# Kernel tuning notes

Hardware: AMD Instinct MI355X
Metric: run time of the kernel (lower is better)

The kernel has to match this reference:

```python
import jax, jax.numpy as jnp
import numpy as np

N_QUBITS = 20
N_BLOCKS = 3
C64 = jnp.complex64


def _u3(theta, phi, lam):
    # U3(theta, phi, lam) = [[cos(t/2), -e^{i lam} sin(t/2)],
    #                        [e^{i phi} sin(t/2), e^{i(phi+lam)} cos(t/2)]]
    ct = jnp.cos(theta / 2).astype(C64)
    st = jnp.sin(theta / 2).astype(C64)
    el = jnp.exp(1j * lam.astype(C64))
    ep = jnp.exp(1j * phi.astype(C64))
    return jnp.stack([jnp.stack([ct, -el * st]),
                      jnp.stack([ep * st, ep * el * ct])])


def _cu3(theta, phi, lam):
    # controlled-U3: identity on control=|0>, U3 on control=|1>
    u = _u3(theta, phi, lam)
    m = jnp.zeros((4, 4), C64)
    m = m.at[:2, :2].set(jnp.eye(2, dtype=C64))
    m = m.at[2:, 2:].set(u)
    return m


def _apply1(psi, m, q):
    # psi: (2,)*N_QUBITS complex state tensor; apply 2x2 gate on qubit q
    psi = jnp.moveaxis(psi, q, 0).reshape(2, -1)
    psi = m @ psi
    return jnp.moveaxis(psi.reshape((2,) * N_QUBITS), 0, q)


def _apply2(psi, m4, c, t):
    # apply 4x4 gate on (control c, target t)
    psi = jnp.moveaxis(psi, (c, t), (0, 1)).reshape(4, -1)
    psi = m4 @ psi
    return jnp.moveaxis(psi.reshape((2,) * N_QUBITS), (0, 1), (c, t))


def _forward(u3_params, cu3_params):
    psi = jnp.zeros((2,) * N_QUBITS, C64).at[(0,) * N_QUBITS].set(1.0)
    for k in range(N_BLOCKS):
        for q in range(N_QUBITS):
            psi = _apply1(psi, _u3(*u3_params[k, q]), q)
        for q in range(N_QUBITS):  # circular CU3 ring: (q, (q+1) % n)
            psi = _apply2(psi, _cu3(*cu3_params[k, q]), q, (q + 1) % N_QUBITS)
    probs = (jnp.abs(psi) ** 2).reshape(2 ** N_QUBITS, 1)
    easy_scale_coeff = 2.0 ** (N_QUBITS - 1)
    gamma, beta, alpha = 0.1, 0.8, 0.3
    x = (beta * jnp.tanh(gamma * easy_scale_coeff * probs)) ** alpha
    return x - jnp.mean(x)


def setup_inputs() -> dict:
    key = jax.random.key(0)
    k1, k2 = jax.random.split(key)
    u3_params = jax.random.normal(k1, (N_BLOCKS, N_QUBITS, 3), dtype=jnp.float32)
    cu3_params = jax.random.normal(k2, (N_BLOCKS, N_QUBITS, 3), dtype=jnp.float32)
    return {"u3_params": u3_params, "cu3_params": cu3_params}


def reference(u3_params, cu3_params):
    return _forward(u3_params, cu3_params)
```

## Files before the change

kernel.cpp:

```cpp
#include <hip/hip_runtime.h>
#include <cstdint>
#include <cstddef>


#define NB 512
#define NT 512
#define SW(i) ((i) ^ (((i) >> 3) & 1u))

__device__ __forceinline__ float2 cmadd2(float2 m0, float2 a0, float2 m1, float2 a1) {
  float2 r;
  r.x = m0.x * a0.x - m0.y * a0.y + m1.x * a1.x - m1.y * a1.y;
  r.y = m0.x * a0.y + m0.y * a0.x + m1.x * a1.y + m1.y * a1.x;
  return r;
}
__device__ __forceinline__ float2 cmul(float2 a, float2 b) {
  return make_float2(a.x * b.x - a.y * b.y, a.x * b.y + a.y * b.x);
}
__device__ __forceinline__ float2 cadd(float2 a, float2 b) {
  return make_float2(a.x + b.x, a.y + b.y);
}

__device__ __forceinline__ void applyU3b0(float2* v, const float2* m) {
  float2 m00 = m[0], m01 = m[1], m10 = m[2], m11 = m[3];
  float2 a0 = v[0], a1 = v[1];
  v[0] = cmadd2(m00, a0, m01, a1); v[1] = cmadd2(m10, a0, m11, a1);
  a0 = v[2]; a1 = v[3];
  v[2] = cmadd2(m00, a0, m01, a1); v[3] = cmadd2(m10, a0, m11, a1);
}
__device__ __forceinline__ void applyF(float2* v, const float2* W0, const float2* W1) {
  float2 a0 = v[0], a1 = v[2];
  v[0] = cmadd2(W0[0], a0, W0[1], a1); v[2] = cmadd2(W0[2], a0, W0[3], a1);
  a0 = v[1]; a1 = v[3];
  v[1] = cmadd2(W1[0], a0, W1[1], a1); v[3] = cmadd2(W1[2], a0, W1[3], a1);
}
__device__ __forceinline__ void applyC(float2* v, const float2* u) {
  float2 a0 = v[1], a1 = v[3];
  v[1] = cmadd2(u[0], a0, u[1], a1); v[3] = cmadd2(u[2], a0, u[3], a1);
}

__device__ __forceinline__ float xval(float2 a) {
  float p = a.x * a.x + a.y * a.y;
  return powf(0.8f * tanhf(52428.8f * p), 0.3f);
}

__device__ __forceinline__ void mat_from(const float* s, float2* m) {
  float st, ct, sl, cl, sp, cp, spl, cpl;
  sincosf(0.5f * s[0], &st, &ct);
  sincosf(s[2], &sl, &cl);
  sincosf(s[1], &sp, &cp);
  sincosf(s[1] + s[2], &spl, &cpl);
  m[0] = make_float2(ct, 0.f);
  m[1] = make_float2(-cl * st, -sl * st);
  m[2] = make_float2(cp * st, sp * st);
  m[3] = make_float2(cpl * ct, spl * ct);
}

template <int TYPE, int INIT, int FINAL>
__global__ __launch_bounds__(NT, 4) void pass_k(const float* __restrict__ u3p,
                                                const float* __restrict__ cu3p, int k,
                                                const float2* __restrict__ in,
                                                float2* __restrict__ outPsi,
                                                float* __restrict__ accum,
                                                float* __restrict__ out) {
  __shared__ float4 A4[1024], B4[1024];
  __shared__ float2 M[168];
  __shared__ float red[8];
  unsigned t = threadIdx.x, b = blockIdx.x;

  float2 v[4];
  if (INIT) {
    v[0] = v[1] = v[2] = v[3] = make_float2(0.f, 0.f);
    if (b == 0 && t == 0) { v[0] = make_float2(1.f, 0.f); *accum = 0.f; }
  } else {
    const float4* in4 = (const float4*)in;
    unsigned F0 = ((t & 255u) << 11) + 2u * (t >> 8) + 4u * (b & 255u) + (b >> 8);
    float4 f0 = in4[F0];
    float4 f1 = in4[F0 + 1024u];
    v[0] = make_float2(f0.x, f0.y); v[1] = make_float2(f0.z, f0.w);
    v[2] = make_float2(f1.x, f1.y); v[3] = make_float2(f1.z, f1.w);
  }

  float2* MU = M;
  float2* MC = M + 80;
  if (t < 20) {
    mat_from(u3p + (k * 20 + t) * 3, MU + 4 * t);
  } else if (t >= 64 && t < 84) {
    unsigned c = t - 64;
    float2 u[4];
    mat_from(cu3p + (k * 20 + c) * 3, u);
    if (c == 19) {
      MC[76] = u[0]; MC[77] = u[1]; MC[78] = u[2]; MC[79] = u[3];
    } else {
      float2 ut[4];
      mat_from(u3p + (k * 20 + c + 1) * 3, ut);
      MC[4 * c + 0] = cadd(cmul(u[0], ut[0]), cmul(u[1], ut[2]));
      MC[4 * c + 1] = cadd(cmul(u[0], ut[1]), cmul(u[1], ut[3]));
      MC[4 * c + 2] = cadd(cmul(u[2], ut[0]), cmul(u[3], ut[2]));
      MC[4 * c + 3] = cadd(cmul(u[2], ut[1]), cmul(u[3], ut[3]));
    }
  }
  __syncthreads();

#pragma unroll
  for (int p = 0; p < 10; ++p) {
    if (TYPE == 0) {
      if (p == 0) applyU3b0(v, MU);
      applyF(v, MU + 4 * (p + 1), MC + 4 * p);
    } else {
      if (p < 9) applyF(v, MU + 4 * (11 + p), MC + 4 * (10 + p));
      else       applyC(v, MC + 4 * 19);
    }
    if (p < 9) {
      float4* buf = (p & 1) ? B4 : A4;
      buf[SW(t)]        = make_float4(v[0].x, v[0].y, v[2].x, v[2].y);
      buf[SW(t + 512u)] = make_float4(v[1].x, v[1].y, v[3].x, v[3].y);
      __syncthreads();
      float4 fa = buf[SW(2u * t)], fb = buf[SW(2u * t + 1u)];
      v[0] = make_float2(fa.x, fa.y); v[1] = make_float2(fa.z, fa.w);
      v[2] = make_float2(fb.x, fb.y); v[3] = make_float2(fb.z, fb.w);
    }
  }

  if (!FINAL) {
    float4* o4 = (float4*)outPsi;
    unsigned F = (b << 10) + 2u * t;
    o4[F]      = make_float4(v[0].x, v[0].y, v[2].x, v[2].y);
    o4[F + 1u] = make_float4(v[1].x, v[1].y, v[3].x, v[3].y);
  } else {
    float xv0 = xval(v[0]), xv1 = xval(v[1]), xv2 = xval(v[2]), xv3 = xval(v[3]);
    float s = xv0 + xv1 + xv2 + xv3;
    float2* o2 = (float2*)out;
    unsigned rt = __brev(t) >> 23, rb = __brev(b) >> 23;
    unsigned base = rt + (rb << 9);
    o2[base] = make_float2(xv0, xv1);
    o2[base + (1u << 18)] = make_float2(xv2, xv3);
#pragma unroll
    for (int o = 32; o > 0; o >>= 1) s += __shfl_down(s, o);
    if ((t & 63u) == 0) red[t >> 6] = s;
    __syncthreads();
    if (t == 0) {
      float tot = 0.f;
#pragma unroll
      for (int i = 0; i < 8; i++) tot += red[i];
      atomicAdd(accum, tot);
    }
  }
}

__global__ void fin_k(float* __restrict__ out, const float* __restrict__ accum) {
  unsigned i = blockIdx.x * blockDim.x + threadIdx.x;
  float mean = *accum * (1.f / 1048576.f);
  float4* o4 = (float4*)out;
  float4 x = o4[i];
  x.x -= mean; x.y -= mean; x.z -= mean; x.w -= mean;
  o4[i] = x;
}

extern "C" void kernel_launch(void* const* d_in, const int* in_sizes, int n_in,
                              void* d_out, int out_size, void* d_ws, size_t ws_size,
                              hipStream_t stream) {
  const float* u3p = (const float*)d_in[0];
  const float* cu3p = (const float*)d_in[1];
  float* out = (float*)d_out;

  char* ws = (char*)d_ws;
  float2* psiA = (float2*)ws;
  float2* psiB = (float2*)(ws + (size_t)8 * 1024 * 1024);
  float* accum = (float*)(ws + (size_t)16 * 1024 * 1024);

  pass_k<0, 1, 0><<<NB, NT, 0, stream>>>(u3p, cu3p, 0, nullptr, psiB, accum, out);
  pass_k<1, 0, 0><<<NB, NT, 0, stream>>>(u3p, cu3p, 0, psiB, psiA, accum, out);
  pass_k<0, 0, 0><<<NB, NT, 0, stream>>>(u3p, cu3p, 1, psiA, psiB, accum, out);
  pass_k<1, 0, 0><<<NB, NT, 0, stream>>>(u3p, cu3p, 1, psiB, psiA, accum, out);
  pass_k<0, 0, 0><<<NB, NT, 0, stream>>>(u3p, cu3p, 2, psiA, psiB, accum, out);
  pass_k<1, 0, 1><<<NB, NT, 0, stream>>>(u3p, cu3p, 2, psiB, nullptr, accum, out);
  fin_k<<<1024, 256, 0, stream>>>(out, accum);
}
```

Before: 140.6 us.

## Use 1024-thread blocks covering 12 qubits per pass with rebalanced gate split

Doubles the block size to 1024 threads and halves the grid, so each block holds 4096 amplitudes (12 qubits) in shared memory. The gate schedule is rebalanced between the two pass types (11 butterfly stages in one, 9 in the other), and the global load/store index mappings and final bit-reversed output indexing change to match. The aim is better-coalesced global access and work spread across more qubits per pass. In exchange it uses larger shared buffers (about 86 KB) and 1024-thread blocks, which lowers occupancy and makes each __syncthreads barrier cost more.

```diff
diff --git a/kernel.cpp b/kernel.cpp
--- a/kernel.cpp
+++ b/kernel.cpp
@@ -3,8 +3,8 @@
 #include <cstddef>
 
 
-#define NB 512
-#define NT 512
+#define NB 256
+#define NT 1024
 #define SW(i) ((i) ^ (((i) >> 3) & 1u))
 
 __device__ __forceinline__ float2 cmadd2(float2 m0, float2 a0, float2 m1, float2 a1) {
@@ -62,9 +62,9 @@
                                                 float2* __restrict__ outPsi,
                                                 float* __restrict__ accum,
                                                 float* __restrict__ out) {
-  __shared__ float4 A4[1024], B4[1024];
+  __shared__ float4 A4[2700], B4[2700];
   __shared__ float2 M[168];
-  __shared__ float red[8];
+  __shared__ float red[16];
   unsigned t = threadIdx.x, b = blockIdx.x;
 
   float2 v[4];
@@ -73,9 +73,14 @@
     if (b == 0 && t == 0) { v[0] = make_float2(1.f, 0.f); *accum = 0.f; }
   } else {
     const float4* in4 = (const float4*)in;
-    unsigned F0 = ((t & 255u) << 11) + 2u * (t >> 8) + 4u * (b & 255u) + (b >> 8);
-    float4 f0 = in4[F0];
-    float4 f1 = in4[F0 + 1024u];
+    unsigned F;
+    if (TYPE == 0)
+      F = ((t >> 7) & 1u) + 2u * ((t >> 8) & 1u) + 4u * ((t >> 9) & 1u) +
+          (b << 3) + ((t & 127u) << 12);
+    else
+      F = ((t >> 9) & 1u) + 2u * ((t >> 7) & 1u) + 4u * ((t >> 8) & 1u) +
+          (b << 3) + ((t & 127u) << 12);
+    float4 f0 = in4[F], f1 = in4[F + 2048u];
     v[0] = make_float2(f0.x, f0.y); v[1] = make_float2(f0.z, f0.w);
     v[2] = make_float2(f1.x, f1.y); v[3] = make_float2(f1.z, f1.w);
   }
@@ -101,19 +106,20 @@
   }
   __syncthreads();
 
+  constexpr int NP = TYPE ? 9 : 11;
 #pragma unroll
-  for (int p = 0; p < 10; ++p) {
+  for (int p = 0; p < NP; ++p) {
     if (TYPE == 0) {
       if (p == 0) applyU3b0(v, MU);
       applyF(v, MU + 4 * (p + 1), MC + 4 * p);
     } else {
-      if (p < 9) applyF(v, MU + 4 * (11 + p), MC + 4 * (10 + p));
+      if (p < 8) applyF(v, MU + 4 * (12 + p), MC + 4 * (11 + p));
       else       applyC(v, MC + 4 * 19);
     }
-    if (p < 9) {
+    if (p < NP - 1 || (TYPE == 1 && !FINAL)) {
       float4* buf = (p & 1) ? B4 : A4;
-      buf[SW(t)]        = make_float4(v[0].x, v[0].y, v[2].x, v[2].y);
-      buf[SW(t + 512u)] = make_float4(v[1].x, v[1].y, v[3].x, v[3].y);
+      buf[SW(t)]         = make_float4(v[0].x, v[0].y, v[2].x, v[2].y);
+      buf[SW(t + 1024u)] = make_float4(v[1].x, v[1].y, v[3].x, v[3].y);
       __syncthreads();
       float4 fa = buf[SW(2u * t)], fb = buf[SW(2u * t + 1u)];
       v[0] = make_float2(fa.x, fa.y); v[1] = make_float2(fa.z, fa.w);
@@ -123,17 +129,25 @@
 
   if (!FINAL) {
     float4* o4 = (float4*)outPsi;
-    unsigned F = (b << 10) + 2u * t;
-    o4[F]      = make_float4(v[0].x, v[0].y, v[2].x, v[2].y);
-    o4[F + 1u] = make_float4(v[1].x, v[1].y, v[3].x, v[3].y);
+    if (TYPE == 0) {
+      unsigned F = 2u * (t & 1u) + 4u * ((t >> 9) & 1u) +
+                   (((t >> 1) & 255u) << 3) + (b << 11);
+      o4[F]      = make_float4(v[0].x, v[0].y, v[2].x, v[2].y);
+      o4[F + 1u] = make_float4(v[1].x, v[1].y, v[3].x, v[3].y);
+    } else {
+      unsigned F = (t << 1) + (b << 11);
+      o4[F]      = make_float4(v[0].x, v[0].y, v[1].x, v[1].y);
+      o4[F + 1u] = make_float4(v[2].x, v[2].y, v[3].x, v[3].y);
+    }
   } else {
     float xv0 = xval(v[0]), xv1 = xval(v[1]), xv2 = xval(v[2]), xv3 = xval(v[3]);
     float s = xv0 + xv1 + xv2 + xv3;
     float2* o2 = (float2*)out;
-    unsigned rt = __brev(t) >> 23, rb = __brev(b) >> 23;
-    unsigned base = rt + (rb << 9);
-    o2[base] = make_float2(xv0, xv1);
-    o2[base + (1u << 18)] = make_float2(xv2, xv3);
+    unsigned rt8 = __brev((t >> 2) & 255u) >> 24;
+    unsigned rb8 = __brev(b & 255u) >> 24;
+    unsigned idx = rt8 + (((t >> 1) & 1u) << 8) + ((t & 1u) << 9) + (rb8 << 10);
+    o2[idx]              = make_float2(xv0, xv1);
+    o2[idx + (1u << 18)] = make_float2(xv2, xv3);
 #pragma unroll
     for (int o = 32; o > 0; o >>= 1) s += __shfl_down(s, o);
     if ((t & 63u) == 0) red[t >> 6] = s;
@@ -141,7 +155,7 @@
     if (t == 0) {
       float tot = 0.f;
 #pragma unroll
-      for (int i = 0; i < 8; i++) tot += red[i];
+      for (int i = 0; i < 16; i++) tot += red[i];
       atomicAdd(accum, tot);
     }
   }
```

Result: no change. 139.0 us (-1.2%).
